# Optimization experiments

Hardware: AMD Instinct MI355X
Metric: run time of the kernel (lower is better)

Reference implementation:

```python
import jax, jax.numpy as jnp
import numpy as np

B, N, F, C, K = 4, 8192, 128, 64, 16


def setup_inputs() -> dict:
    key = jax.random.key(0)
    ks = jax.random.split(key, 24)
    s = 0.05
    rn = lambda k, shape: (jax.random.normal(k, shape, jnp.float32) * s)
    return {
        "features": jax.random.normal(ks[0], (B, N, F), jnp.float32),
        "positions": jax.random.normal(ks[1], (B, N, 3), jnp.float32),
        "batch": jnp.repeat(jnp.arange(B, dtype=jnp.int32), N),
        "num_neighbors": K,
        # linear encoder (F -> C)
        "W_enc": rn(ks[2], (F, C)), "b_enc": jnp.zeros((C,), jnp.float32),
        # point-transformer q/k/v projections (C -> C)
        "Wq": rn(ks[3], (C, C)), "bq": jnp.zeros((C,), jnp.float32),
        "Wk": rn(ks[4], (C, C)), "bk": jnp.zeros((C,), jnp.float32),
        "Wv": rn(ks[5], (C, C)), "bv": jnp.zeros((C,), jnp.float32),
        # positional encoding MLP: 3 -> C -> C (ReLU)
        "Wp1": rn(ks[6], (3, C)), "bp1": jnp.zeros((C,), jnp.float32),
        "Wp2": rn(ks[7], (C, C)), "bp2": jnp.zeros((C,), jnp.float32),
        # attention MLP gamma: C -> C -> C (ReLU)
        "Wa1": rn(ks[8], (C, C)), "ba1": jnp.zeros((C,), jnp.float32),
        "Wa2": rn(ks[9], (C, C)), "ba2": jnp.zeros((C,), jnp.float32),
        # linear decoder (C -> F)
        "W_dec": rn(ks[10], (C, F)), "b_dec": jnp.zeros((F,), jnp.float32),
    }


def reference(features, positions, batch, num_neighbors,
              W_enc, b_enc, Wq, bq, Wk, bk, Wv, bv,
              Wp1, bp1, Wp2, bp2, Wa1, ba1, Wa2, ba2, W_dec, b_dec):
    # linear encode: [B,N,F] -> [B,N,C]
    x = features @ W_enc + b_enc
    q = x @ Wq + bq
    k = x @ Wk + bk
    v = x @ Wv + bv

    def per_cloud(pos, qi, ki, vi):
        # kNN via pairwise squared distances (self included, dist 0)
        sq = jnp.sum(pos * pos, axis=-1)                      # [N]
        d2 = sq[:, None] + sq[None, :] - 2.0 * (pos @ pos.T)  # [N,N]
        idx = jax.lax.top_k(-d2, num_neighbors)[1]            # [N,K]
        kj = ki[idx]                                          # [N,K,C] gather
        vj = vi[idx]                                          # [N,K,C]
        rel = pos[:, None, :] - pos[idx]                      # [N,K,3]
        # positional encoding delta = MLP(p_i - p_j)
        delta = jax.nn.relu(rel @ Wp1 + bp1) @ Wp2 + bp2      # [N,K,C]
        # vector attention: gamma(q_i - k_j + delta), softmax over K neighbors
        a = qi[:, None, :] - kj + delta
        a = jax.nn.relu(a @ Wa1 + ba1) @ Wa2 + ba2
        w = jax.nn.softmax(a, axis=1)                         # [N,K,C]
        return jnp.sum(w * (vj + delta), axis=1)              # [N,C]

    y = jax.vmap(per_cloud)(positions, q, k, v)               # [B,N,C]
    out = y @ W_dec + b_dec + features                        # decode + residual
    return (out, positions, batch)
```

## Files before the change

### kernel.cpp

```cpp
#include <hip/hip_runtime.h>
#include <hip/hip_bf16.h>

#define NPTS 32768
#define NPC  8192
#define KNN  16
#define CH   64
#define FDIM 128
#define EMPTYKEY 0x7F7FFFFFu

typedef __bf16 bf16;
typedef __bf16 bf16x2 __attribute__((ext_vector_type(2)));
typedef __bf16 bf16x8 __attribute__((ext_vector_type(8)));
typedef float  f32x4  __attribute__((ext_vector_type(4)));

__global__ __launch_bounds__(256) void k_encode(
    const float* __restrict__ feat,
    const float* __restrict__ Wenc, const float* __restrict__ benc,
    const float* __restrict__ Wq, const float* __restrict__ bq,
    const float* __restrict__ Wk, const float* __restrict__ bk,
    const float* __restrict__ Wv, const float* __restrict__ bv,
    bf16* __restrict__ qo, bf16* __restrict__ kvo)
{
    __shared__ float xs[4][CH];
    int t = threadIdx.x;
    int c = t & 63, pl = t >> 6;
    size_t pt = (size_t)blockIdx.x * 4 + pl;
    const float* fr = feat + pt * FDIM;
    float acc = benc[c];
#pragma unroll 8
    for (int f4 = 0; f4 < 32; ++f4) {
        float4 fv = *reinterpret_cast<const float4*>(fr + f4 * 4);
        acc += fv.x * Wenc[(f4*4+0)*CH + c];
        acc += fv.y * Wenc[(f4*4+1)*CH + c];
        acc += fv.z * Wenc[(f4*4+2)*CH + c];
        acc += fv.w * Wenc[(f4*4+3)*CH + c];
    }
    xs[pl][c] = acc;
    __syncthreads();
    float aq = bq[c], ak = bk[c], av = bv[c];
#pragma unroll 4
    for (int m = 0; m < CH; ++m) {
        float xm = xs[pl][m];
        aq += xm * Wq[m*CH + c];
        ak += xm * Wk[m*CH + c];
        av += xm * Wv[m*CH + c];
    }
    qo[pt*CH + c] = (bf16)aq;
    bf16x2 kv2; kv2[0] = (bf16)ak; kv2[1] = (bf16)av;
    *reinterpret_cast<bf16x2*>(&kvo[pt*2*CH + 2*c]) = kv2;
}

__global__ __launch_bounds__(256, 4) void k_knn(
    const float* __restrict__ pos, unsigned* __restrict__ wsK)
{
    __shared__ float4 sp[1024];
    __shared__ unsigned sbuf[256 * 17];

    int t = threadIdx.x;
    int blk = blockIdx.x;
    int slice = blk & 7;
    int qg = (blk >> 3) & 31;
    int cloud = blk >> 8;
    const float* pc = pos + (size_t)cloud * NPC * 3;
    int jbase = slice << 10;

    {
        const float4* src = reinterpret_cast<const float4*>(pc + (size_t)jbase * 3);
        float4 a = src[t*3+0], b1 = src[t*3+1], c1 = src[t*3+2];
        sp[t*4+0] = make_float4(a.x,  a.y,  a.z,  0.f);
        sp[t*4+1] = make_float4(a.w,  b1.x, b1.y, 0.f);
        sp[t*4+2] = make_float4(b1.z, b1.w, c1.x, 0.f);
        sp[t*4+3] = make_float4(c1.y, c1.z, c1.w, 0.f);
    }
    __syncthreads();

    int qi = (qg << 8) + t;
    float myx = pc[qi*3+0], myy = pc[qi*3+1], myz = pc[qi*3+2];

    unsigned arr[16];
#pragma unroll
    for (int r = 0; r < 16; ++r) arr[r] = EMPTYKEY;
    float thrf = __uint_as_float(EMPTYKEY & 0xFFFFE000u);
    int cnt = 0;
    int base = t * 17;

    for (int g = 0; g < 1024; g += 4) {
        float d2v[4];
#pragma unroll
        for (int u = 0; u < 4; ++u) {
            float4 p = sp[g + u];
            float dx = myx - p.x, dy = myy - p.y, dz = myz - p.z;
            d2v[u] = dx*dx + dy*dy + dz*dz;
        }
        float m4 = fminf(fminf(d2v[0], d2v[1]), fminf(d2v[2], d2v[3]));
        if (__any(m4 <= thrf)) {
#pragma unroll
            for (int u = 0; u < 4; ++u) {
                if (d2v[u] <= thrf) {
                    sbuf[base + cnt] = (__float_as_uint(d2v[u]) & 0xFFFFE000u)
                                       | (unsigned)(jbase + g + u);
                    ++cnt;
                }
            }
            if (__any(cnt >= 13)) {
#pragma unroll
                for (int b = 0; b < 16; ++b) {
                    unsigned key = (b < cnt) ? sbuf[base + b] : EMPTYKEY;
                    if (key < arr[15]) {
#pragma unroll
                        for (int r = 0; r < 16; ++r) {
                            unsigned lo = min(key, arr[r]);
                            unsigned hi = max(key, arr[r]);
                            arr[r] = lo; key = hi;
                        }
                    }
                }
                cnt = 0;
                thrf = __uint_as_float(arr[15] & 0xFFFFE000u);
            }
        }
    }
#pragma unroll
    for (int b = 0; b < 16; ++b) {
        unsigned key = (b < cnt) ? sbuf[base + b] : EMPTYKEY;
        if (key < arr[15]) {
#pragma unroll
            for (int r = 0; r < 16; ++r) {
                unsigned lo = min(key, arr[r]);
                unsigned hi = max(key, arr[r]);
                arr[r] = lo; key = hi;
            }
        }
    }
    size_t gq = (size_t)cloud * NPC + qi;
#pragma unroll
    for (int r = 0; r < 16; ++r) wsK[(size_t)(slice*16 + r)*NPTS + gq] = arr[r];
}

__global__ __launch_bounds__(64) void k_merge(
    const unsigned* __restrict__ wsK, int* __restrict__ idxout,
    const float* __restrict__ Wp2, const float* __restrict__ Wa1,
    const float* __restrict__ Wa2, bf16* __restrict__ wpk)
{
    __shared__ unsigned kk[64][137];
    int t = threadIdx.x;
    size_t q = (size_t)blockIdx.x * 64 + t;
#pragma unroll
    for (int l = 0; l < 8; ++l) {
#pragma unroll
        for (int r = 0; r < 16; ++r)
            kk[t][l*17 + r] = wsK[(size_t)(l*16 + r)*NPTS + q];
        kk[t][l*17 + 16] = 0xFFFFFFFFu;
    }

    unsigned h0=0,h1=0,h2=0,h3=0,h4=0,h5=0,h6=0,h7=0;
    int* o = idxout + q * KNN;
    for (int r = 0; r < KNN; ++r) {
        unsigned best = 0xFFFFFFFFu; int bl = 0; unsigned k;
        k = kk[t][0*17 + h0]; if (k < best) { best = k; bl = 0; }
        k = kk[t][1*17 + h1]; if (k < best) { best = k; bl = 1; }
        k = kk[t][2*17 + h2]; if (k < best) { best = k; bl = 2; }
        k = kk[t][3*17 + h3]; if (k < best) { best = k; bl = 3; }
        k = kk[t][4*17 + h4]; if (k < best) { best = k; bl = 4; }
        k = kk[t][5*17 + h5]; if (k < best) { best = k; bl = 5; }
        k = kk[t][6*17 + h6]; if (k < best) { best = k; bl = 6; }
        k = kk[t][7*17 + h7]; if (k < best) { best = k; bl = 7; }
        o[r] = (int)(best & 0x1FFFu);
        h0 += (bl == 0); h1 += (bl == 1); h2 += (bl == 2); h3 += (bl == 3);
        h4 += (bl == 4); h5 += (bl == 5); h6 += (bl == 6); h7 += (bl == 7);
    }

    if (blockIdx.x == 0) {
        int lane = t;
        int mlane = lane & 15, kgrp = lane >> 4;
        const float* Ws[3] = {Wp2, Wa1, Wa2};
        bf16x8* ow = reinterpret_cast<bf16x8*>(wpk);
        for (int gmm = 0; gmm < 3; ++gmm) {
#pragma unroll
            for (int nt = 0; nt < 4; ++nt) {
#pragma unroll
                for (int kt = 0; kt < 2; ++kt) {
                    bf16x8 v;
#pragma unroll
                    for (int j = 0; j < 8; ++j)
                        v[j] = (bf16)Ws[gmm][(kt*32 + kgrp*8 + j)*CH + nt*16 + mlane];
                    ow[(gmm*8 + nt*2 + kt)*64 + lane] = v;
                }
            }
        }
    }
}

__device__ __forceinline__ void wave_gemm(
    const bf16* At, f32x4 acc[4][4], const bf16x8* __restrict__ wpk,
    int w, int lane)
{
    int kgrp = lane >> 4;
    bf16x8 wf[4][2];
#pragma unroll
    for (int nt = 0; nt < 4; ++nt)
#pragma unroll
        for (int kt = 0; kt < 2; ++kt)
            wf[nt][kt] = wpk[(nt*2 + kt)*64 + lane];
#pragma unroll
    for (int mt = 0; mt < 4; ++mt) {
        int row = w*64 + mt*16 + (lane & 15);
        const bf16* rb = At + row*CH;
        int sw = row & 7;
        bf16x8 a0 = *reinterpret_cast<const bf16x8*>(rb + ((kgrp     ^ sw) * 8));
        bf16x8 a1 = *reinterpret_cast<const bf16x8*>(rb + (((4+kgrp) ^ sw) * 8));
#pragma unroll
        for (int nt = 0; nt < 4; ++nt) {
            acc[mt][nt] = __builtin_amdgcn_mfma_f32_16x16x32_bf16(a0, wf[nt][0], acc[mt][nt], 0, 0, 0);
            acc[mt][nt] = __builtin_amdgcn_mfma_f32_16x16x32_bf16(a1, wf[nt][1], acc[mt][nt], 0, 0, 0);
        }
    }
}

__global__ __launch_bounds__(128, 3) void k_attn(
    const float* __restrict__ pos, const int* __restrict__ nidx,
    const bf16* __restrict__ qg, const bf16* __restrict__ kvg,
    const float* __restrict__ Wp1, const float* __restrict__ bp1,
    const float* __restrict__ bp2, const float* __restrict__ ba1,
    const float* __restrict__ ba2, const bf16* __restrict__ wpkg,
    float* __restrict__ yout)
{
    __shared__ bf16 At[128 * CH];

    int t = threadIdx.x;
    int w = t >> 6, lane = t & 63;
    int mlane = lane & 15, kgrp = lane >> 4;
    int blk = blockIdx.x;
    int xcd = blk & 7;
    int cloud = xcd >> 1;
    int sub = ((blk >> 3) << 1) | (xcd & 1);
    size_t cbase = (size_t)cloud * NPC;
    size_t p0 = cbase + (size_t)sub * 8;
    const bf16x2* kv2 = reinterpret_cast<const bf16x2*>(kvg);
    const bf16x8* wpk = reinterpret_cast<const bf16x8*>(wpkg);

    {
        int p = t >> 4, j = t & 15;
        size_t gp = p0 + p;
        int nbr = nidx[gp*KNN + j];
        size_t gn = cbase + (size_t)nbr;
        float rx = pos[gp*3+0] - pos[gn*3+0];
        float ry = pos[gp*3+1] - pos[gn*3+1];
        float rz = pos[gp*3+2] - pos[gn*3+2];
        float h[CH];
#pragma unroll
        for (int c4 = 0; c4 < 16; ++c4) {
            float4 w0 = *reinterpret_cast<const float4*>(Wp1 + 0*CH + c4*4);
            float4 w1 = *reinterpret_cast<const float4*>(Wp1 + 1*CH + c4*4);
            float4 w2 = *reinterpret_cast<const float4*>(Wp1 + 2*CH + c4*4);
            float4 bb = *reinterpret_cast<const float4*>(bp1 + c4*4);
            h[c4*4+0] = fmaxf(rx*w0.x + ry*w1.x + rz*w2.x + bb.x, 0.f);
            h[c4*4+1] = fmaxf(rx*w0.y + ry*w1.y + rz*w2.y + bb.y, 0.f);
            h[c4*4+2] = fmaxf(rx*w0.z + ry*w1.z + rz*w2.z + bb.z, 0.f);
            h[c4*4+3] = fmaxf(rx*w0.w + ry*w1.w + rz*w2.w + bb.w, 0.f);
        }
#pragma unroll
        for (int ch = 0; ch < 8; ++ch) {
            bf16x8 v;
#pragma unroll
            for (int e = 0; e < 8; ++e) v[e] = (bf16)h[ch*8 + e];
            *reinterpret_cast<bf16x8*>(&At[t*CH + (ch ^ (t & 7)) * 8]) = v;
        }
    }

    f32x4 acc[4][4];

#pragma unroll
    for (int nt = 0; nt < 4; ++nt) {
        float b = bp2[nt*16 + mlane];
#pragma unroll
        for (int mt = 0; mt < 4; ++mt) { acc[mt][nt][0]=b; acc[mt][nt][1]=b; acc[mt][nt][2]=b; acc[mt][nt][3]=b; }
    }
    wave_gemm(At, acc, wpk, w, lane);

    bf16x2 vdp[4][4][2];
#pragma unroll
    for (int mt = 0; mt < 4; ++mt) {
        size_t gp = p0 + (size_t)(w*4 + mt);
        int nb[4];
#pragma unroll
        for (int reg = 0; reg < 4; ++reg)
            nb[reg] = nidx[gp*KNN + kgrp*4 + reg];
#pragma unroll
        for (int nt = 0; nt < 4; ++nt) {
            int c = nt*16 + mlane;
            float qv = (float)qg[gp*CH + c];
            float vdf[4];
#pragma unroll
            for (int reg = 0; reg < 4; ++reg) {
                float dlt = acc[mt][nt][reg];
                size_t gr = cbase + (size_t)nb[reg];
                bf16x2 kvp = kv2[gr*CH + c];
                float kvf = (float)kvp[0];
                float vv  = (float)kvp[1];
                int row = w*64 + mt*16 + kgrp*4 + reg;
                int off = row*CH + (((c >> 3) ^ (row & 7)) * 8) + (c & 7);
                At[off] = (bf16)(qv - kvf + dlt);
                vdf[reg] = vv + dlt;
            }
            bf16x2 lo2; lo2[0] = (bf16)vdf[0]; lo2[1] = (bf16)vdf[1];
            bf16x2 hi2; hi2[0] = (bf16)vdf[2]; hi2[1] = (bf16)vdf[3];
            vdp[mt][nt][0] = lo2;
            vdp[mt][nt][1] = hi2;
        }
    }

#pragma unroll
    for (int nt = 0; nt < 4; ++nt) {
        float b = ba1[nt*16 + mlane];
#pragma unroll
        for (int mt = 0; mt < 4; ++mt) { acc[mt][nt][0]=b; acc[mt][nt][1]=b; acc[mt][nt][2]=b; acc[mt][nt][3]=b; }
    }
    wave_gemm(At, acc, wpk + 512, w, lane);
#pragma unroll
    for (int mt = 0; mt < 4; ++mt) {
#pragma unroll
        for (int nt = 0; nt < 4; ++nt) {
            int c = nt*16 + mlane;
#pragma unroll
            for (int reg = 0; reg < 4; ++reg) {
                int row = w*64 + mt*16 + kgrp*4 + reg;
                int off = row*CH + (((c >> 3) ^ (row & 7)) * 8) + (c & 7);
                At[off] = (bf16)fmaxf(acc[mt][nt][reg], 0.f);
            }
        }
    }

#pragma unroll
    for (int nt = 0; nt < 4; ++nt) {
        float b = ba2[nt*16 + mlane];
#pragma unroll
        for (int mt = 0; mt < 4; ++mt) { acc[mt][nt][0]=b; acc[mt][nt][1]=b; acc[mt][nt][2]=b; acc[mt][nt][3]=b; }
    }
    wave_gemm(At, acc, wpk + 1024, w, lane);

#pragma unroll
    for (int mt = 0; mt < 4; ++mt) {
        size_t gp = p0 + (size_t)(w*4 + mt);
#pragma unroll
        for (int nt = 0; nt < 4; ++nt) {
            int c = nt*16 + mlane;
            float m = fmaxf(fmaxf(acc[mt][nt][0], acc[mt][nt][1]),
                            fmaxf(acc[mt][nt][2], acc[mt][nt][3]));
            m = fmaxf(m, __shfl_xor(m, 16));
            m = fmaxf(m, __shfl_xor(m, 32));
            float e[4], s = 0.f;
#pragma unroll
            for (int reg = 0; reg < 4; ++reg) { e[reg] = __expf(acc[mt][nt][reg] - m); s += e[reg]; }
            s += __shfl_xor(s, 16);
            s += __shfl_xor(s, 32);
            float num = 0.f;
            num += e[0] * (float)vdp[mt][nt][0][0];
            num += e[1] * (float)vdp[mt][nt][0][1];
            num += e[2] * (float)vdp[mt][nt][1][0];
            num += e[3] * (float)vdp[mt][nt][1][1];
            num += __shfl_xor(num, 16);
            num += __shfl_xor(num, 32);
            if (kgrp == 0) yout[gp*CH + c] = num / s;
        }
    }
}

__global__ __launch_bounds__(256) void k_decode(
    const float* __restrict__ y, const float* __restrict__ Wd, const float* __restrict__ bd,
    const float* __restrict__ feat, const float* __restrict__ pos,
    const int* __restrict__ batch, float* __restrict__ out)
{
    int t = threadIdx.x;
    int f = t & 127, pl = t >> 7;
    size_t pt = (size_t)blockIdx.x * 2 + pl;
    const float* yr = y + pt*CH;
    float acc = bd[f] + feat[pt*FDIM + f];
#pragma unroll
    for (int c4 = 0; c4 < 16; ++c4) {
        float4 yv = *reinterpret_cast<const float4*>(yr + c4*4);
        acc += yv.x * Wd[(c4*4+0)*FDIM + f];
        acc += yv.y * Wd[(c4*4+1)*FDIM + f];
        acc += yv.z * Wd[(c4*4+2)*FDIM + f];
        acc += yv.w * Wd[(c4*4+3)*FDIM + f];
    }
    out[pt*FDIM + f] = acc;

    int i = blockIdx.x * 256 + t;
    if (i < NPTS*3) out[(size_t)NPTS*FDIM + i] = pos[i];
    if (i < NPTS)   out[(size_t)NPTS*FDIM + NPTS*3 + i] = (float)batch[i];
}

extern "C" void kernel_launch(void* const* d_in, const int* in_sizes, int n_in,
                              void* d_out, int out_size, void* d_ws, size_t ws_size,
                              hipStream_t stream)
{
    const float* feat  = (const float*)d_in[0];
    const float* pos   = (const float*)d_in[1];
    const int*   batch = (const int*)d_in[2];
    const float* Wenc  = (const float*)d_in[4];
    const float* benc  = (const float*)d_in[5];
    const float* Wq = (const float*)d_in[6];   const float* bq = (const float*)d_in[7];
    const float* Wk = (const float*)d_in[8];   const float* bk = (const float*)d_in[9];
    const float* Wv = (const float*)d_in[10];  const float* bv = (const float*)d_in[11];
    const float* Wp1= (const float*)d_in[12];  const float* bp1= (const float*)d_in[13];
    const float* Wp2= (const float*)d_in[14];  const float* bp2= (const float*)d_in[15];
    const float* Wa1= (const float*)d_in[16];  const float* ba1= (const float*)d_in[17];
    const float* Wa2= (const float*)d_in[18];  const float* ba2= (const float*)d_in[19];
    const float* Wd = (const float*)d_in[20];  const float* bd = (const float*)d_in[21];
    float* out = (float*)d_out;

    int*      idx = (int*)d_ws;
    unsigned* wsK = (unsigned*)((char*)d_ws + (size_t)NPTS*KNN*sizeof(int));
    bf16* qb  = (bf16*)wsK;
    bf16* kvb = qb + (size_t)NPTS*CH;
    float* yb = (float*)((char*)wsK + (size_t)NPTS*KNN*8*sizeof(unsigned));
    bf16*  wpk = (bf16*)(yb + (size_t)NPTS*CH);

    k_knn<<<1024, 256, 0, stream>>>(pos, wsK);
    k_merge<<<NPTS/64, 64, 0, stream>>>(wsK, idx, Wp2, Wa1, Wa2, wpk);

    k_encode<<<NPTS/4, 256, 0, stream>>>(feat, Wenc, benc, Wq, bq, Wk, bk, Wv, bv, qb, kvb);

    k_attn<<<NPTS/8, 128, 0, stream>>>(pos, idx, qb, kvb,
                                       Wp1, bp1, bp2, ba1, ba2, wpk, yb);

    k_decode<<<NPTS/2, 256, 0, stream>>>(yb, Wd, bd, feat, pos, batch, out);
}
```

Before: 465.3 us.

## Sort points by Morton code per cloud to improve neighbor gather locality

Adds a per-cloud bitonic sort of points by 3D Morton code, then runs kNN, encoding and attention in sorted order with permutation and inverse-permutation arrays. Nearby points become nearby in memory, so neighbor gathers of k/v and positions in the attention kernel should hit cache more often. The block-to-point mapping in attention is changed so each XCD handles a contiguous range. The cost is an extra single-block-per-cloud sort kernel and indirect reads in encode and decode.

Result: slower. 727.8 us (+56.4%).

```diff
diff --git a/kernel.cpp b/kernel.cpp
--- a/kernel.cpp
+++ b/kernel.cpp
@@ -13,8 +13,61 @@
 typedef __bf16 bf16x8 __attribute__((ext_vector_type(8)));
 typedef float  f32x4  __attribute__((ext_vector_type(4)));
 
+__device__ __forceinline__ unsigned spread3(unsigned v) {
+    v &= 0x3FFu;
+    v = (v | (v << 16)) & 0x030000FFu;
+    v = (v | (v << 8))  & 0x0300F00Fu;
+    v = (v | (v << 4))  & 0x030C30C3u;
+    v = (v | (v << 2))  & 0x09249249u;
+    return v;
+}
+
+__global__ __launch_bounds__(1024) void k_sort(
+    const float* __restrict__ pos, int* __restrict__ perm,
+    int* __restrict__ invperm, float* __restrict__ posS)
+{
+    __shared__ unsigned keys[NPC];
+    int cloud = blockIdx.x;
+    int t = threadIdx.x;
+    int cb = cloud * NPC;
+    const float* pc = pos + (size_t)cb * 3;
+
+    for (int i = t; i < NPC; i += 1024) {
+        float x = pc[i*3+0], y = pc[i*3+1], z = pc[i*3+2];
+        int xi = (int)((x + 4.f) * 8.f); xi = xi < 0 ? 0 : (xi > 63 ? 63 : xi);
+        int yi = (int)((y + 4.f) * 8.f); yi = yi < 0 ? 0 : (yi > 63 ? 63 : yi);
+        int zi = (int)((z + 4.f) * 8.f); zi = zi < 0 ? 0 : (zi > 63 ? 63 : zi);
+        unsigned m = (spread3((unsigned)xi) << 2) | (spread3((unsigned)yi) << 1) | spread3((unsigned)zi);
+        keys[i] = (m << 13) | (unsigned)i;
+    }
+    __syncthreads();
+
+    for (unsigned k = 2; k <= NPC; k <<= 1) {
+        for (unsigned j = k >> 1; j > 0; j >>= 1) {
+            for (int i = t; i < NPC; i += 1024) {
+                int ixj = i ^ (int)j;
+                if (ixj > i) {
+                    unsigned a = keys[i], b = keys[ixj];
+                    bool up = ((i & (int)k) == 0);
+                    if ((a > b) == up) { keys[i] = b; keys[ixj] = a; }
+                }
+            }
+            __syncthreads();
+        }
+    }
+
+    for (int s = t; s < NPC; s += 1024) {
+        int l = (int)(keys[s] & 0x1FFFu);
+        perm[cb + s] = cb + l;
+        invperm[cb + l] = cb + s;
+        posS[(size_t)(cb + s)*3 + 0] = pc[l*3+0];
+        posS[(size_t)(cb + s)*3 + 1] = pc[l*3+1];
+        posS[(size_t)(cb + s)*3 + 2] = pc[l*3+2];
+    }
+}
+
 __global__ __launch_bounds__(256) void k_encode(
-    const float* __restrict__ feat,
+    const float* __restrict__ feat, const int* __restrict__ perm,
     const float* __restrict__ Wenc, const float* __restrict__ benc,
     const float* __restrict__ Wq, const float* __restrict__ bq,
     const float* __restrict__ Wk, const float* __restrict__ bk,
@@ -25,7 +78,8 @@
     int t = threadIdx.x;
     int c = t & 63, pl = t >> 6;
     size_t pt = (size_t)blockIdx.x * 4 + pl;
-    const float* fr = feat + pt * FDIM;
+    size_t orig = (size_t)perm[pt];
+    const float* fr = feat + orig * FDIM;
     float acc = benc[c];
 #pragma unroll 8
     for (int f4 = 0; f4 < 32; ++f4) {
@@ -192,7 +246,7 @@
 }
 
 __device__ __forceinline__ void wave_gemm(
-    const bf16* At, f32x4 acc[4][4], const bf16x8* __restrict__ wpk,
+    const bf16* At, f32x4 (&acc)[4][4], const bf16x8* __restrict__ wpk,
     int w, int lane)
 {
     int kgrp = lane >> 4;
@@ -230,12 +284,10 @@
     int t = threadIdx.x;
     int w = t >> 6, lane = t & 63;
     int mlane = lane & 15, kgrp = lane >> 4;
-    int blk = blockIdx.x;
-    int xcd = blk & 7;
-    int cloud = xcd >> 1;
-    int sub = ((blk >> 3) << 1) | (xcd & 1);
-    size_t cbase = (size_t)cloud * NPC;
-    size_t p0 = cbase + (size_t)sub * 8;
+    int blk0 = blockIdx.x;
+    int blk = ((blk0 & 7) << 9) | (blk0 >> 3);
+    size_t p0 = (size_t)blk * 8;
+    size_t cbase = (p0 >> 13) << 13;
     const bf16x2* kv2 = reinterpret_cast<const bf16x2*>(kvg);
     const bf16x8* wpk = reinterpret_cast<const bf16x8*>(wpkg);
 
@@ -367,14 +419,15 @@
 }
 
 __global__ __launch_bounds__(256) void k_decode(
-    const float* __restrict__ y, const float* __restrict__ Wd, const float* __restrict__ bd,
+    const float* __restrict__ y, const int* __restrict__ invperm,
+    const float* __restrict__ Wd, const float* __restrict__ bd,
     const float* __restrict__ feat, const float* __restrict__ pos,
     const int* __restrict__ batch, float* __restrict__ out)
 {
     int t = threadIdx.x;
     int f = t & 127, pl = t >> 7;
     size_t pt = (size_t)blockIdx.x * 2 + pl;
-    const float* yr = y + pt*CH;
+    const float* yr = y + (size_t)invperm[pt]*CH;
     float acc = bd[f] + feat[pt*FDIM + f];
 #pragma unroll
     for (int c4 = 0; c4 < 16; ++c4) {
@@ -410,20 +463,25 @@
     const float* Wd = (const float*)d_in[20];  const float* bd = (const float*)d_in[21];
     float* out = (float*)d_out;
 
-    int*      idx = (int*)d_ws;
-    unsigned* wsK = (unsigned*)((char*)d_ws + (size_t)NPTS*KNN*sizeof(int));
+    char* W = (char*)d_ws;
+    int*      idx = (int*)W;
+    unsigned* wsK = (unsigned*)(W + (size_t)NPTS*KNN*4);
     bf16* qb  = (bf16*)wsK;
     bf16* kvb = qb + (size_t)NPTS*CH;
-    float* yb = (float*)((char*)wsK + (size_t)NPTS*KNN*8*sizeof(unsigned));
+    float* yb = (float*)(W + (size_t)NPTS*KNN*4 + (size_t)NPTS*KNN*8*4);
     bf16*  wpk = (bf16*)(yb + (size_t)NPTS*CH);
-
-    k_knn<<<1024, 256, 0, stream>>>(pos, wsK);
+    int*   perm    = (int*)((char*)wpk + 32768);
+    int*   invperm = perm + NPTS;
+    float* posS    = (float*)(invperm + NPTS);
+
+    k_sort<<<4, 1024, 0, stream>>>(pos, perm, invperm, posS);
+    k_knn<<<1024, 256, 0, stream>>>(posS, wsK);
     k_merge<<<NPTS/64, 64, 0, stream>>>(wsK, idx, Wp2, Wa1, Wa2, wpk);
 
-    k_encode<<<NPTS/4, 256, 0, stream>>>(feat, Wenc, benc, Wq, bq, Wk, bk, Wv, bv, qb, kvb);
-
-    k_attn<<<NPTS/8, 128, 0, stream>>>(pos, idx, qb, kvb,
+    k_encode<<<NPTS/4, 256, 0, stream>>>(feat, perm, Wenc, benc, Wq, bq, Wk, bk, Wv, bv, qb, kvb);
+
+    k_attn<<<NPTS/8, 128, 0, stream>>>(posS, idx, qb, kvb,
                                        Wp1, bp1, bp2, ba1, ba2, wpk, yb);
 
-    k_decode<<<NPTS/2, 256, 0, stream>>>(yb, Wd, bd, feat, pos, batch, out);
-}
+    k_decode<<<NPTS/2, 256, 0, stream>>>(yb, invperm, Wd, bd, feat, pos, batch, out);
+}
```
